# Kernel optimization log

Hardware: AMD Instinct MI355X
Metric: run time of the kernel (lower is better)

## Reference

```python
import jax, jax.numpy as jnp
import numpy as np

B, S, HID = 2, 2048, 1024
NH, NKV = 16, 4
HD = HID // NH          # 64
NREP = NH // NKV        # 4
EPS = 1e-06


def _rotate_half(x):
    h = x.shape[-1] // 2
    return jnp.concatenate([-x[..., h:], x[..., :h]], axis=-1)


def _rope(q, k, cos, sin):
    # q: [b,s,h,d], k: [b,s,kv,d]; cos/sin: [s,d] -> unsqueeze head dim
    c = cos[:, None, :]
    s = sin[:, None, :]
    return q * c + _rotate_half(q) * s, k * c + _rotate_half(k) * s


def setup_inputs() -> dict:
    key = jax.random.key(0)
    ks = jax.random.split(key, 8)
    sc = 0.02
    return {
        "x": jax.random.normal(ks[0], (B, S, HID), jnp.float32),
        "cos": jnp.cos(jnp.arange(S, dtype=jnp.float32)[:, None] *
                       (1.0 / (1e6 ** (jnp.arange(HD, dtype=jnp.float32) / HD)))),
        "sin": jnp.sin(jnp.arange(S, dtype=jnp.float32)[:, None] *
                       (1.0 / (1e6 ** (jnp.arange(HD, dtype=jnp.float32) / HD)))),
        "attention_mask": jnp.ones((B, S), jnp.int32),
        "Wq": jax.random.normal(ks[1], (HID, NH * HD), jnp.float32) * sc,
        "Wk": jax.random.normal(ks[2], (HID, NKV * HD), jnp.float32) * sc,
        "Wv": jax.random.normal(ks[3], (HID, NKV * HD), jnp.float32) * sc,
        "Wo": jax.random.normal(ks[4], (NH * HD, HID), jnp.float32) * sc,
    }


def reference(x, cos, sin, attention_mask, Wq, Wk, Wv, Wo):
    b, s, _ = x.shape
    q = (x @ Wq).reshape(b, s, NH, HD)
    k = (x @ Wk).reshape(b, s, NKV, HD)
    v = (x @ Wv).reshape(b, s, NKV, HD)
    q, k = _rope(q, k, cos[:s], sin[:s])
    # GQA repeat: [b,s,kv,d] -> [b,s,h,d]
    k = jnp.repeat(k, NREP, axis=2)
    v = jnp.repeat(v, NREP, axis=2)
    # -> [b,h,s,d]
    q = jnp.transpose(q, (0, 2, 1, 3))
    k = jnp.transpose(k, (0, 2, 1, 3))
    v = jnp.transpose(v, (0, 2, 1, 3))
    # feature map: elu(x) + 1 (positive features)
    q = jax.nn.elu(q) + 1.0
    k = jax.nn.elu(k) + 1.0
    # prefill path (seq_len > 1): non-causal kernelized scores
    scores = jnp.einsum("bhsd,bhtd->bhst", q, k)  # [b,h,s,s]
    mask = attention_mask[:, None, None, :]       # [b,1,1,s]
    scores = jnp.where(mask == 0, 0.0, scores)
    denom = jnp.clip(
        jax.lax.stop_gradient(jnp.abs(scores).sum(-1, keepdims=True)), 1e-06, None)
    scores = scores / denom
    out = jnp.einsum("bhst,bhtd->bhsd", scores, v)
    out = jnp.transpose(out, (0, 2, 1, 3)).reshape(b, s, NH * HD)
    return out @ Wo
```

## Files before the change

kernel.cpp:

```cpp
#include <hip/hip_runtime.h>
#include <hip/hip_bf16.h>

using u16 = unsigned short;
using u32 = unsigned int;

namespace {
constexpr int S   = 2048;
constexpr int HID = 1024;
constexpr int M   = 4096;
constexpr int K   = 1024;
}

typedef __attribute__((ext_vector_type(8))) short short8;
typedef __attribute__((ext_vector_type(4))) float f32x4;

__device__ __forceinline__ u16 f2bf(float f) {
    u32 u = __builtin_bit_cast(u32, f);
    u += 0x7fffu + ((u >> 16) & 1u);
    return (u16)(u >> 16);
}
__device__ __forceinline__ float bf2f(u16 h) {
    return __builtin_bit_cast(float, (u32)h << 16);
}
__device__ __forceinline__ float phi(float x) {
    return x > 0.f ? x + 1.f : __expf(x);
}
__device__ __forceinline__ void glds16(const u16* g, u16* l) {
    __builtin_amdgcn_global_load_lds(
        (const __attribute__((address_space(1))) u32*)g,
        (__attribute__((address_space(3))) u32*)l, 16, 0, 0);
}

template <int MODE>
__global__ __launch_bounds__(256, 2) void gemm_k(
    const u16* __restrict__ A, const u16* __restrict__ B,
    u16* __restrict__ Cq, float* __restrict__ Ckv,
    float* __restrict__ Cf, int ldc, int zAr, int zBr, int zCr,
    const float* __restrict__ Cos, const float* __restrict__ Sin,
    const int* __restrict__ Mask)
{
    constexpr int BK = 32;
    constexpr int NT = K / BK;
    __shared__ __align__(16) u16 sA0[128 * BK], sA1[128 * BK];
    __shared__ __align__(16) u16 sB0[128 * BK], sB1[128 * BK];

    A += (size_t)blockIdx.z * zAr * K;
    B += (size_t)blockIdx.z * zBr * K;
    if (MODE == 1) Cf += (size_t)blockIdx.z * zCr * ldc;

    const int tid  = threadIdx.x;
    const int lane = tid & 63, w = tid >> 6;
    const int wm = w & 1, wn = w >> 1;
    const int m0 = blockIdx.x * 128, n0 = blockIdx.y * 128;
    const int fr = lane & 15, fq = lane >> 4;

    const int str = lane >> 2;
    const int stk = ((lane & 3) ^ ((lane >> 3) & 3)) * 8;

    const u16* Ab = A + (size_t)(m0 + w * 32 + str) * K + stk;
    const u16* Bb = B + (size_t)(n0 + w * 32 + str) * K + stk;
    const int lo0 = (w * 32) * BK, lo1 = (w * 32 + 16) * BK;

    f32x4 acc[4][4] = {};
    const int kswz = (fq ^ ((fr >> 1) & 3)) * 8;

#define STAGE(dA, dB, kt)                                   \
    do {                                                    \
        glds16(Ab + (kt),              dA + lo0);           \
        glds16(Ab + (size_t)16 * K + (kt), dA + lo1);       \
        glds16(Bb + (kt),              dB + lo0);           \
        glds16(Bb + (size_t)16 * K + (kt), dB + lo1);       \
    } while (0)

#define COMPUTE(sAc, sBc)                                                   \
    do {                                                                    \
        short8 ah[4], bh[4];                                                \
        _Pragma("unroll")                                                   \
        for (int i = 0; i < 4; ++i) {                                       \
            ah[i] = *(const short8*)(sAc + (wm * 64 + i * 16 + fr) * BK + kswz); \
            bh[i] = *(const short8*)(sBc + (wn * 64 + i * 16 + fr) * BK + kswz); \
        }                                                                   \
        _Pragma("unroll")                                                   \
        for (int i = 0; i < 4; ++i)                                         \
            _Pragma("unroll")                                               \
            for (int j = 0; j < 4; ++j)                                     \
                acc[i][j] = __builtin_amdgcn_mfma_f32_16x16x32_bf16(        \
                    ah[i], bh[j], acc[i][j], 0, 0, 0);                      \
    } while (0)

#define SYNC()                                              \
    do {                                                    \
        asm volatile("s_waitcnt vmcnt(0)" ::: "memory");    \
        __syncthreads();                                    \
    } while (0)

    STAGE(sA0, sB0, 0);
    SYNC();
    for (int t = 0; t < NT; t += 2) {
        if (t + 1 < NT) STAGE(sA1, sB1, (t + 1) * BK);
        COMPUTE(sA0, sB0);
        SYNC();
        if (t + 2 < NT) STAGE(sA0, sB0, (t + 2) * BK);
        COMPUTE(sA1, sB1);
        SYNC();
    }
#undef STAGE
#undef COMPUTE
#undef SYNC

    const bool isQ = (MODE == 0) && (n0 < 1024);
    const bool isK = (MODE == 0) && (n0 >= 1024) && (n0 < 1280);
#pragma unroll
    for (int i = 0; i < 4; ++i)
#pragma unroll
        for (int jj = 0; jj < 4; ++jj) {
            const int row = m0 + wm * 64 + i * 16 + fq * 4 + jj;
            float v0 = acc[i][0][jj], v1 = acc[i][1][jj];
            float v2 = acc[i][2][jj], v3 = acc[i][3][jj];
            if (MODE == 1) {
                float* cr = &Cf[(size_t)row * ldc + n0 + wn * 64 + fr];
                cr[0] = v0; cr[16] = v1; cr[32] = v2; cr[48] = v3;
                continue;
            }
            if (isQ || isK) {
                const int sb = (row & (S - 1)) * 64;
                float r0 = v0 * Cos[sb + fr]      - v2 * Sin[sb + fr];
                float r2 = v2 * Cos[sb + fr + 32] + v0 * Sin[sb + fr + 32];
                float r1 = v1 * Cos[sb + fr + 16] - v3 * Sin[sb + fr + 16];
                float r3 = v3 * Cos[sb + fr + 48] + v1 * Sin[sb + fr + 48];
                v0 = phi(r0); v1 = phi(r1); v2 = phi(r2); v3 = phi(r3);
            }
            if (isQ) {
                u16* cr = &Cq[(size_t)row * 1024 + n0 + wn * 64 + fr];
                cr[0]  = f2bf(v0); cr[16] = f2bf(v1);
                cr[32] = f2bf(v2); cr[48] = f2bf(v3);
            } else if (isK) {
                const float mv = (float)Mask[row];
                float* cr = &Ckv[(size_t)row * 512 + (n0 - 1024) + wn * 64 + fr];
                cr[0] = v0 * mv; cr[16] = v1 * mv;
                cr[32] = v2 * mv; cr[48] = v3 * mv;
            } else {
                float* cr = &Ckv[(size_t)row * 512 + 256 + (n0 - 1280) + wn * 64 + fr];
                cr[0] = v0; cr[16] = v1; cr[32] = v2; cr[48] = v3;
            }
        }
}

__global__ __launch_bounds__(256) void split_x_k(
    const float* __restrict__ X, u16* __restrict__ H)
{
    const int i = (blockIdx.x * 256 + threadIdx.x) * 4;
    float4 v = *reinterpret_cast<const float4*>(&X[i]);
    ushort4 h;
    h.x = f2bf(v.x);
    h.y = f2bf(v.y);
    h.z = f2bf(v.z);
    h.w = f2bf(v.w);
    *reinterpret_cast<ushort4*>(&H[i]) = h;
}

__global__ __launch_bounds__(256) void wsplit_k(
    const float* __restrict__ W, int N,
    u16* __restrict__ Th, int nbase)
{
    __shared__ float t[32][33];
    const int n0 = blockIdx.x * 32, k0 = blockIdx.y * 32;
    const int tx = threadIdx.x, ty = threadIdx.y;
#pragma unroll
    for (int i = 0; i < 4; ++i)
        t[ty + i * 8][tx] = W[(size_t)(k0 + ty + i * 8) * N + n0 + tx];
    __syncthreads();
#pragma unroll
    for (int i = 0; i < 4; ++i) {
        const int n = ty + i * 8;
        Th[(size_t)(nbase + n0 + n) * 1024 + k0 + tx] = f2bf(t[tx][n]);
    }
}

__global__ __launch_bounds__(256) void kv_stage1_k(
    const float* __restrict__ KVf, float* __restrict__ part)
{
    const int g  = blockIdx.x;
    const int ch = blockIdx.y;
    const int b  = g >> 2, kvh = g & 3;
    const int tid = threadIdx.x;

    __shared__ float ks[64][64];
    __shared__ float vs[64][64];
    const int m0 = b * S + ch * 64;
#pragma unroll
    for (int l = 0; l < 4; ++l) {
        int idx = tid + l * 256;
        int r = idx >> 4, q4 = (idx & 15) * 4;
        const float* src = KVf + (size_t)(m0 + r) * 512 + kvh * 64;
        *reinterpret_cast<float4*>(&ks[r][q4]) = *reinterpret_cast<const float4*>(src + q4);
        *reinterpret_cast<float4*>(&vs[r][q4]) = *reinterpret_cast<const float4*>(src + 256 + q4);
    }
    __syncthreads();

    const int i = tid >> 2, j0 = (tid & 3) * 16;
    float4 a0 = {0,0,0,0}, a1 = {0,0,0,0}, a2 = {0,0,0,0}, a3 = {0,0,0,0};
#pragma unroll 8
    for (int r = 0; r < 64; ++r) {
        float kv = ks[r][i];
        float4 w0 = *reinterpret_cast<const float4*>(&vs[r][j0]);
        float4 w1 = *reinterpret_cast<const float4*>(&vs[r][j0 + 4]);
        float4 w2 = *reinterpret_cast<const float4*>(&vs[r][j0 + 8]);
        float4 w3 = *reinterpret_cast<const float4*>(&vs[r][j0 + 12]);
        a0.x = fmaf(kv, w0.x, a0.x); a0.y = fmaf(kv, w0.y, a0.y);
        a0.z = fmaf(kv, w0.z, a0.z); a0.w = fmaf(kv, w0.w, a0.w);
        a1.x = fmaf(kv, w1.x, a1.x); a1.y = fmaf(kv, w1.y, a1.y);
        a1.z = fmaf(kv, w1.z, a1.z); a1.w = fmaf(kv, w1.w, a1.w);
        a2.x = fmaf(kv, w2.x, a2.x); a2.y = fmaf(kv, w2.y, a2.y);
        a2.z = fmaf(kv, w2.z, a2.z); a2.w = fmaf(kv, w2.w, a2.w);
        a3.x = fmaf(kv, w3.x, a3.x); a3.y = fmaf(kv, w3.y, a3.y);
        a3.z = fmaf(kv, w3.z, a3.z); a3.w = fmaf(kv, w3.w, a3.w);
    }
    float* dst = part + ((size_t)g * 32 + ch) * 4160;
    float* d0 = dst + i * 64 + j0;
    *reinterpret_cast<float4*>(d0)      = a0;
    *reinterpret_cast<float4*>(d0 + 4)  = a1;
    *reinterpret_cast<float4*>(d0 + 8)  = a2;
    *reinterpret_cast<float4*>(d0 + 12) = a3;
    if (tid < 64) {
        float ksum = 0.f;
#pragma unroll 8
        for (int r = 0; r < 64; ++r) ksum += ks[r][tid];
        dst[4096 + tid] = ksum;
    }
}

__global__ __launch_bounds__(256) void kv_reduce_k(
    const float* __restrict__ part, u16* __restrict__ KVh,
    float* __restrict__ Ksumf)
{
    const int g = blockIdx.x;
    const int e = blockIdx.y * 256 + threadIdx.x;
    if (e >= 4160) return;
    const float* p = part + (size_t)g * 32 * 4160 + e;
    float s = 0.f;
#pragma unroll 8
    for (int c = 0; c < 32; ++c) s += p[(size_t)c * 4160];
    if (e < 4096) KVh[g * 4096 + e] = f2bf(s);
    else          Ksumf[g * 64 + (e - 4096)] = s;
}

__global__ __launch_bounds__(256, 2) void kw_gemm_k(
    const u16* __restrict__ WoT, const u16* __restrict__ KVb,
    u16* __restrict__ KWT)
{
    __shared__ __align__(16) u16 sA[128 * 64];
    __shared__ __align__(16) u16 sB[64 * 64];

    const int tid = threadIdx.x, lane = tid & 63, w = tid >> 6;
    const int o0 = blockIdx.x * 128;
    const int gh = blockIdx.y, b = gh >> 4, h = gh & 15, g = b * 4 + (h >> 2);
    const int fr = lane & 15, fq = lane >> 4;
    const int srow = lane >> 3, sslot = lane & 7;
    const int sswz = (sslot ^ srow) * 8;

#pragma unroll
    for (int c = 0; c < 4; ++c) {
        const int rb = w * 32 + c * 8;
        glds16(WoT + (size_t)(o0 + rb + srow) * 1024 + h * 64 + sswz, sA + rb * 64);
    }
#pragma unroll
    for (int c = 0; c < 2; ++c) {
        const int rb = w * 16 + c * 8;
        glds16(KVb + (size_t)g * 4096 + (rb + srow) * 64 + sswz, sB + rb * 64);
    }
    asm volatile("s_waitcnt vmcnt(0)" ::: "memory");
    __syncthreads();

    f32x4 acc[2][4] = {};
#pragma unroll
    for (int kk = 0; kk < 2; ++kk) {
        short8 a_h[2], b_h[4];
#pragma unroll
        for (int i = 0; i < 2; ++i) {
            const int row = w * 32 + i * 16 + fr;
            a_h[i] = *(const short8*)(sA + row * 64 + ((kk * 4 + fq) ^ (fr & 7)) * 8);
        }
#pragma unroll
        for (int j = 0; j < 4; ++j) {
            const int row = j * 16 + fr;
            b_h[j] = *(const short8*)(sB + row * 64 + ((kk * 4 + fq) ^ (fr & 7)) * 8);
        }
#pragma unroll
        for (int i = 0; i < 2; ++i)
#pragma unroll
            for (int j = 0; j < 4; ++j)
                acc[i][j] = __builtin_amdgcn_mfma_f32_16x16x32_bf16(
                    a_h[i], b_h[j], acc[i][j], 0, 0, 0);
    }
#pragma unroll
    for (int i = 0; i < 2; ++i)
#pragma unroll
        for (int j = 0; j < 4; ++j)
#pragma unroll
            for (int jj = 0; jj < 4; ++jj) {
                const int row = o0 + w * 32 + i * 16 + fq * 4 + jj;
                const int col = j * 16 + fr;
                KWT[((size_t)b * 1024 + row) * 1024 + h * 64 + col] =
                    f2bf(acc[i][j][jj]);
            }
}

__global__ __launch_bounds__(256) void qhat_k(
    const u16* __restrict__ Qt, const float* __restrict__ Ksumf,
    u16* __restrict__ Qh)
{
    const int t = blockIdx.x * 256 + threadIdx.x;
    const int m = t >> 4, h = t & 15;
    const int g = (m >> 11) * 4 + (h >> 2);
    const u16* q  = Qt + (size_t)m * 1024 + h * 64;
    const float* Ks = Ksumf + g * 64;

    float qv[64];
    float den = 0.f;
#pragma unroll
    for (int c = 0; c < 8; ++c) {
        short8 v8 = *reinterpret_cast<const short8*>(q + c * 8);
#pragma unroll
        for (int j = 0; j < 8; ++j) {
            qv[c * 8 + j] = bf2f((u16)v8[j]);
            den = fmaf(qv[c * 8 + j], Ks[c * 8 + j], den);
        }
    }
    const float rd = 1.f / fmaxf(den, 1e-6f);
    u16* o = Qh + (size_t)m * 1024 + h * 64;
#pragma unroll
    for (int c = 0; c < 8; ++c) {
        short8 ov;
#pragma unroll
        for (int j = 0; j < 8; ++j) ov[j] = (short)f2bf(qv[c * 8 + j] * rd);
        *reinterpret_cast<short8*>(o + c * 8) = ov;
    }
}

extern "C" void kernel_launch(void* const* d_in, const int* in_sizes, int n_in,
                              void* d_out, int out_size, void* d_ws, size_t ws_size,
                              hipStream_t stream)
{
    const float* x    = (const float*)d_in[0];
    const float* cosp = (const float*)d_in[1];
    const float* sinp = (const float*)d_in[2];
    const int*   msk  = (const int*)d_in[3];
    const float* Wq   = (const float*)d_in[4];
    const float* Wk   = (const float*)d_in[5];
    const float* Wv   = (const float*)d_in[6];
    const float* Wo   = (const float*)d_in[7];
    float* out = (float*)d_out;

    u16* xbf  = (u16*)d_ws;
    u16* wt   = xbf  + (size_t)M * K;
    u16* wot  = wt   + (size_t)1536 * K;
    u16* qt   = wot  + (size_t)K * K;
    u16* qhat = qt   + (size_t)M * K;
    u16* kvb  = qhat + (size_t)M * K;
    u16* kwt  = kvb  + 8 * 4096;
    float* kvf   = (float*)(kwt + (size_t)2 * K * K);
    float* part  = kvf + (size_t)M * 512;
    float* ksumf = part + (size_t)8 * 32 * 4160;

    split_x_k<<<(M * K) / 1024, 256, 0, stream>>>(x, xbf);
    dim3 wb(32, 8);
    wsplit_k<<<dim3(32, 32), wb, 0, stream>>>(Wq, 1024, wt, 0);
    wsplit_k<<<dim3(8, 32),  wb, 0, stream>>>(Wk, 256,  wt, 1024);
    wsplit_k<<<dim3(8, 32),  wb, 0, stream>>>(Wv, 256,  wt, 1280);
    wsplit_k<<<dim3(32, 32), wb, 0, stream>>>(Wo, 1024, wot, 0);

    gemm_k<0><<<dim3(M / 128, 1536 / 128, 1), 256, 0, stream>>>(
        xbf, wt, qt, kvf, nullptr, 0, 0, 0, 0, cosp, sinp, msk);

    kv_stage1_k<<<dim3(8, 32), 256, 0, stream>>>(kvf, part);
    kv_reduce_k<<<dim3(8, 17), 256, 0, stream>>>(part, kvb, ksumf);

    kw_gemm_k<<<dim3(8, 32), 256, 0, stream>>>(wot, kvb, kwt);

    qhat_k<<<(M * 16) / 256, 256, 0, stream>>>(qt, ksumf, qhat);

    gemm_k<1><<<dim3(2048 / 128, HID / 128, 2), 256, 0, stream>>>(
        qhat, kwt, nullptr, nullptr, out, HID, 2048, 1024, 2048,
        nullptr, nullptr, nullptr);
}
```

Before: 85.07 us.

## Retile GEMM to 64x128 with BK=64 and fuse prep kernels into one launch

The GEMM kernel moves from 128x128 tiles with BK=32 to 64x128 tiles with BK=64. It uses a new XOR swizzle for LDS staging and allows 3 blocks per CU instead of 2, which doubles the grid so more CUs stay busy. The four weight-transpose kernels and the x-to-bf16 conversion are merged into one prep kernel to cut launch overhead. In exchange, the smaller M tile means more B-matrix traffic per output, and the tighter launch bound may limit registers.

```diff
diff --git a/kernel.cpp b/kernel.cpp
--- a/kernel.cpp
+++ b/kernel.cpp
@@ -32,16 +32,16 @@
 }
 
 template <int MODE>
-__global__ __launch_bounds__(256, 2) void gemm_k(
+__global__ __launch_bounds__(256, 3) void gemm_k(
     const u16* __restrict__ A, const u16* __restrict__ B,
     u16* __restrict__ Cq, float* __restrict__ Ckv,
     float* __restrict__ Cf, int ldc, int zAr, int zBr, int zCr,
     const float* __restrict__ Cos, const float* __restrict__ Sin,
     const int* __restrict__ Mask)
 {
-    constexpr int BK = 32;
+    constexpr int BK = 64;
     constexpr int NT = K / BK;
-    __shared__ __align__(16) u16 sA0[128 * BK], sA1[128 * BK];
+    __shared__ __align__(16) u16 sA0[64 * BK],  sA1[64 * BK];
     __shared__ __align__(16) u16 sB0[128 * BK], sB1[128 * BK];
 
     A += (size_t)blockIdx.z * zAr * K;
@@ -51,41 +51,48 @@
     const int tid  = threadIdx.x;
     const int lane = tid & 63, w = tid >> 6;
     const int wm = w & 1, wn = w >> 1;
-    const int m0 = blockIdx.x * 128, n0 = blockIdx.y * 128;
+    const int m0 = blockIdx.x * 64, n0 = blockIdx.y * 128;
     const int fr = lane & 15, fq = lane >> 4;
 
-    const int str = lane >> 2;
-    const int stk = ((lane & 3) ^ ((lane >> 3) & 3)) * 8;
-
-    const u16* Ab = A + (size_t)(m0 + w * 32 + str) * K + stk;
-    const u16* Bb = B + (size_t)(n0 + w * 32 + str) * K + stk;
-    const int lo0 = (w * 32) * BK, lo1 = (w * 32 + 16) * BK;
-
-    f32x4 acc[4][4] = {};
-    const int kswz = (fq ^ ((fr >> 1) & 3)) * 8;
-
-#define STAGE(dA, dB, kt)                                   \
-    do {                                                    \
-        glds16(Ab + (kt),              dA + lo0);           \
-        glds16(Ab + (size_t)16 * K + (kt), dA + lo1);       \
-        glds16(Bb + (kt),              dB + lo0);           \
-        glds16(Bb + (size_t)16 * K + (kt), dB + lo1);       \
+    const int srow  = lane >> 3;
+    const int sslot = lane & 7;
+    const int sswz  = (sslot ^ srow) * 8;
+
+    const u16* Asrc = A + (size_t)(m0 + w * 8 + srow) * K + sswz;
+    const u16* Bsrc = B + (size_t)(n0 + w * 8 + srow) * K + sswz;
+    const int ldsb = (w * 8) * BK;
+
+    f32x4 acc[2][4] = {};
+
+#define STAGE(dA, dB, kt)                                          \
+    do {                                                           \
+        glds16(Asrc + (kt),                 dA + ldsb);            \
+        glds16(Asrc + (size_t)32 * K + (kt), dA + 32 * BK + ldsb); \
+        glds16(Bsrc + (kt),                 dB + ldsb);            \
+        glds16(Bsrc + (size_t)32 * K + (kt), dB + 32 * BK + ldsb); \
+        glds16(Bsrc + (size_t)64 * K + (kt), dB + 64 * BK + ldsb); \
+        glds16(Bsrc + (size_t)96 * K + (kt), dB + 96 * BK + ldsb); \
     } while (0)
 
-#define COMPUTE(sAc, sBc)                                                   \
-    do {                                                                    \
-        short8 ah[4], bh[4];                                                \
-        _Pragma("unroll")                                                   \
-        for (int i = 0; i < 4; ++i) {                                       \
-            ah[i] = *(const short8*)(sAc + (wm * 64 + i * 16 + fr) * BK + kswz); \
-            bh[i] = *(const short8*)(sBc + (wn * 64 + i * 16 + fr) * BK + kswz); \
-        }                                                                   \
-        _Pragma("unroll")                                                   \
-        for (int i = 0; i < 4; ++i)                                         \
-            _Pragma("unroll")                                               \
-            for (int j = 0; j < 4; ++j)                                     \
-                acc[i][j] = __builtin_amdgcn_mfma_f32_16x16x32_bf16(        \
-                    ah[i], bh[j], acc[i][j], 0, 0, 0);                      \
+#define COMPUTE(sAc, sBc)                                                    \
+    do {                                                                     \
+        _Pragma("unroll")                                                    \
+        for (int kk = 0; kk < 2; ++kk) {                                     \
+            const int ks = ((kk * 4 + fq) ^ (fr & 7)) * 8;                   \
+            short8 ah[2], bh[4];                                             \
+            _Pragma("unroll")                                                \
+            for (int i = 0; i < 2; ++i)                                      \
+                ah[i] = *(const short8*)(sAc + (wm * 32 + i * 16 + fr) * BK + ks); \
+            _Pragma("unroll")                                                \
+            for (int j = 0; j < 4; ++j)                                      \
+                bh[j] = *(const short8*)(sBc + (wn * 64 + j * 16 + fr) * BK + ks); \
+            _Pragma("unroll")                                                \
+            for (int i = 0; i < 2; ++i)                                      \
+                _Pragma("unroll")                                            \
+                for (int j = 0; j < 4; ++j)                                  \
+                    acc[i][j] = __builtin_amdgcn_mfma_f32_16x16x32_bf16(     \
+                        ah[i], bh[j], acc[i][j], 0, 0, 0);                   \
+        }                                                                    \
     } while (0)
 
 #define SYNC()                                              \
@@ -96,6 +103,7 @@
 
     STAGE(sA0, sB0, 0);
     SYNC();
+#pragma unroll 1
     for (int t = 0; t < NT; t += 2) {
         if (t + 1 < NT) STAGE(sA1, sB1, (t + 1) * BK);
         COMPUTE(sA0, sB0);
@@ -111,10 +119,10 @@
     const bool isQ = (MODE == 0) && (n0 < 1024);
     const bool isK = (MODE == 0) && (n0 >= 1024) && (n0 < 1280);
 #pragma unroll
-    for (int i = 0; i < 4; ++i)
+    for (int i = 0; i < 2; ++i)
 #pragma unroll
         for (int jj = 0; jj < 4; ++jj) {
-            const int row = m0 + wm * 64 + i * 16 + fq * 4 + jj;
+            const int row = m0 + wm * 32 + i * 16 + fq * 4 + jj;
             float v0 = acc[i][0][jj], v1 = acc[i][1][jj];
             float v2 = acc[i][2][jj], v3 = acc[i][3][jj];
             if (MODE == 1) {
@@ -146,26 +154,31 @@
         }
 }
 
-__global__ __launch_bounds__(256) void split_x_k(
-    const float* __restrict__ X, u16* __restrict__ H)
-{
-    const int i = (blockIdx.x * 256 + threadIdx.x) * 4;
-    float4 v = *reinterpret_cast<const float4*>(&X[i]);
-    ushort4 h;
-    h.x = f2bf(v.x);
-    h.y = f2bf(v.y);
-    h.z = f2bf(v.z);
-    h.w = f2bf(v.w);
-    *reinterpret_cast<ushort4*>(&H[i]) = h;
-}
-
-__global__ __launch_bounds__(256) void wsplit_k(
-    const float* __restrict__ W, int N,
-    u16* __restrict__ Th, int nbase)
-{
+__global__ __launch_bounds__(256) void prep_k(
+    const float* __restrict__ X,  u16* __restrict__ Xb,
+    const float* __restrict__ Wq, const float* __restrict__ Wk,
+    const float* __restrict__ Wv, const float* __restrict__ Wo,
+    u16* __restrict__ wt, u16* __restrict__ wot)
+{
+    const int bid = blockIdx.x, tid = threadIdx.x;
+    if (bid < 4096) {
+        const int i = (bid * 256 + tid) * 4;
+        float4 v = *reinterpret_cast<const float4*>(&X[i]);
+        ushort4 h;
+        h.x = f2bf(v.x); h.y = f2bf(v.y); h.z = f2bf(v.z); h.w = f2bf(v.w);
+        *reinterpret_cast<ushort4*>(&Xb[i]) = h;
+        return;
+    }
+    int r = bid - 4096;
+    const float* W; u16* T; int N, nbase, bx, by;
+    if (r < 1024)      { W = Wq; T = wt;  N = 1024; nbase = 0;    bx = r & 31; by = r >> 5; }
+    else if (r < 1280) { r -= 1024; W = Wk; T = wt; N = 256; nbase = 1024; bx = r & 7; by = r >> 3; }
+    else if (r < 1536) { r -= 1280; W = Wv; T = wt; N = 256; nbase = 1280; bx = r & 7; by = r >> 3; }
+    else               { r -= 1536; W = Wo; T = wot; N = 1024; nbase = 0;  bx = r & 31; by = r >> 5; }
+
     __shared__ float t[32][33];
-    const int n0 = blockIdx.x * 32, k0 = blockIdx.y * 32;
-    const int tx = threadIdx.x, ty = threadIdx.y;
+    const int n0 = bx * 32, k0 = by * 32;
+    const int tx = tid & 31, ty = tid >> 5;
 #pragma unroll
     for (int i = 0; i < 4; ++i)
         t[ty + i * 8][tx] = W[(size_t)(k0 + ty + i * 8) * N + n0 + tx];
@@ -173,7 +186,7 @@
 #pragma unroll
     for (int i = 0; i < 4; ++i) {
         const int n = ty + i * 8;
-        Th[(size_t)(nbase + n0 + n) * 1024 + k0 + tx] = f2bf(t[tx][n]);
+        T[(size_t)(nbase + n0 + n) * 1024 + k0 + tx] = f2bf(t[tx][n]);
     }
 }
 
@@ -363,14 +376,10 @@
     float* part  = kvf + (size_t)M * 512;
     float* ksumf = part + (size_t)8 * 32 * 4160;
 
-    split_x_k<<<(M * K) / 1024, 256, 0, stream>>>(x, xbf);
-    dim3 wb(32, 8);
-    wsplit_k<<<dim3(32, 32), wb, 0, stream>>>(Wq, 1024, wt, 0);
-    wsplit_k<<<dim3(8, 32),  wb, 0, stream>>>(Wk, 256,  wt, 1024);
-    wsplit_k<<<dim3(8, 32),  wb, 0, stream>>>(Wv, 256,  wt, 1280);
-    wsplit_k<<<dim3(32, 32), wb, 0, stream>>>(Wo, 1024, wot, 0);
-
-    gemm_k<0><<<dim3(M / 128, 1536 / 128, 1), 256, 0, stream>>>(
+    prep_k<<<4096 + 1024 + 256 + 256 + 1024, 256, 0, stream>>>(
+        x, xbf, Wq, Wk, Wv, Wo, wt, wot);
+
+    gemm_k<0><<<dim3(M / 64, 1536 / 128, 1), 256, 0, stream>>>(
         xbf, wt, qt, kvf, nullptr, 0, 0, 0, 0, cosp, sinp, msk);
 
     kv_stage1_k<<<dim3(8, 32), 256, 0, stream>>>(kvf, part);
@@ -380,7 +389,7 @@
 
     qhat_k<<<(M * 16) / 256, 256, 0, stream>>>(qt, ksumf, qhat);
 
-    gemm_k<1><<<dim3(2048 / 128, HID / 128, 2), 256, 0, stream>>>(
+    gemm_k<1><<<dim3(2048 / 64, HID / 128, 2), 256, 0, stream>>>(
         qhat, kwt, nullptr, nullptr, out, HID, 2048, 1024, 2048,
         nullptr, nullptr, nullptr);
 }
```

After: 70.14 us, median of 2. 17.6% less time.
